# Performance work log

Measured on AMD Instinct MI355X. Metric: run time of the kernel, lower is better.

The kernel has to match this reference:

```python
import jax, jax.numpy as jnp
import numpy as np

B, QL, CL = 4, 256, 512
XD, ED, DIM, YD = 128, 128, 128, 16


def setup_inputs() -> dict:
    key = jax.random.key(0)
    ks = jax.random.split(key, 9)
    s = lambda fan_in: 1.0 / np.sqrt(fan_in)
    return {
        "q": jax.random.normal(ks[0], (B, QL, XD), jnp.float32),
        "f_embed": jax.random.normal(ks[1], (B, CL, ED), jnp.float32),
        "att_logits": jax.random.normal(ks[2], (B, QL, CL), jnp.float32),
        # layer 1 of concat-MLP, split into per-branch blocks (same math as concat@W1)
        "W1q": jax.random.normal(ks[3], (XD, DIM), jnp.float32) * s(XD + ED),
        "W1f": jax.random.normal(ks[4], (ED, DIM), jnp.float32) * s(XD + ED),
        "b1": jnp.zeros((DIM,), jnp.float32),
        "W2": jax.random.normal(ks[5], (DIM, DIM), jnp.float32) * s(DIM),
        "b2": jnp.zeros((DIM,), jnp.float32),
        "Wout": jax.random.normal(ks[6], (DIM, 2 * YD), jnp.float32) * s(DIM),
        "bout": jnp.zeros((2 * YD,), jnp.float32),
    }


def reference(q, f_embed, att_logits, W1q, W1f, b1, W2, b2, Wout, bout):
    # First layer: concat([tile(q), tile(f)]) @ W1 == q@W1q (+) f@W1f broadcast-added.
    qp = jnp.einsum("bqd,dh->bqh", q, W1q)            # [B,Q,H]
    fp = jnp.einsum("bcd,dh->bch", f_embed, W1f)      # [B,C,H]
    h = jax.nn.relu(qp[:, :, None, :] + fp[:, None, :, :] + b1)   # [B,Q,C,H]
    h = jax.nn.relu(jnp.einsum("bqch,hk->bqck", h, W2) + b2)      # [B,Q,C,H]
    out = jnp.einsum("bqch,hy->bqcy", h, Wout) + bout             # [B,Q,C,2Y]
    mu, s = jnp.split(out, 2, axis=-1)                            # [B,Q,C,Y] each
    sigma = jax.nn.softplus(jnp.maximum(-15.0, s))
    # MixtureSameFamily(Categorical(att_logits), MVNDiag(mu, sigma)).sample()
    kcat, keps = jax.random.split(jax.random.key(1))
    idx = jax.random.categorical(kcat, att_logits, axis=-1)       # [B,Q]
    gather = lambda t: jnp.take_along_axis(t, idx[:, :, None, None], axis=2)[:, :, 0, :]
    mu_sel, sig_sel = gather(mu), gather(sigma)                   # [B,Q,Y]
    eps = jax.random.normal(keps, mu_sel.shape, mu_sel.dtype)
    y_hat = mu_sel + sig_sel * eps                                # [B,Q,Y]
    return y_hat
```

## Files before the change

kernel.cpp:

```cpp
#include <hip/hip_runtime.h>
#include <stdint.h>

#define Bc   4
#define QLc  256
#define CLc  512
#define Dc   128
#define YDc  16
#define NROW (Bc * QLc)

__device__ __forceinline__ uint32_t rotl32(uint32_t x, int d) {
  return (x << d) | (x >> (32 - d));
}

__device__ __forceinline__ void tf2x32(uint32_t k0, uint32_t k1, uint32_t x0,
                                       uint32_t x1, uint32_t& o0, uint32_t& o1) {
  const uint32_t k2 = k0 ^ k1 ^ 0x1BD11BDAu;
  uint32_t v0 = x0 + k0, v1 = x1 + k1;
  v0 += v1; v1 = rotl32(v1, 13); v1 ^= v0;
  v0 += v1; v1 = rotl32(v1, 15); v1 ^= v0;
  v0 += v1; v1 = rotl32(v1, 26); v1 ^= v0;
  v0 += v1; v1 = rotl32(v1, 6);  v1 ^= v0;
  v0 += k1; v1 += k2 + 1u;
  v0 += v1; v1 = rotl32(v1, 17); v1 ^= v0;
  v0 += v1; v1 = rotl32(v1, 29); v1 ^= v0;
  v0 += v1; v1 = rotl32(v1, 16); v1 ^= v0;
  v0 += v1; v1 = rotl32(v1, 24); v1 ^= v0;
  v0 += k2; v1 += k0 + 2u;
  v0 += v1; v1 = rotl32(v1, 13); v1 ^= v0;
  v0 += v1; v1 = rotl32(v1, 15); v1 ^= v0;
  v0 += v1; v1 = rotl32(v1, 26); v1 ^= v0;
  v0 += v1; v1 = rotl32(v1, 6);  v1 ^= v0;
  v0 += k0; v1 += k1 + 3u;
  v0 += v1; v1 = rotl32(v1, 17); v1 ^= v0;
  v0 += v1; v1 = rotl32(v1, 29); v1 ^= v0;
  v0 += v1; v1 = rotl32(v1, 16); v1 ^= v0;
  v0 += v1; v1 = rotl32(v1, 24); v1 ^= v0;
  v0 += k1; v1 += k2 + 4u;
  v0 += v1; v1 = rotl32(v1, 13); v1 ^= v0;
  v0 += v1; v1 = rotl32(v1, 15); v1 ^= v0;
  v0 += v1; v1 = rotl32(v1, 26); v1 ^= v0;
  v0 += v1; v1 = rotl32(v1, 6);  v1 ^= v0;
  v0 += k2; v1 += k0 + 5u;
  o0 = v0; o1 = v1;
}

__device__ __forceinline__ void subkeys(uint32_t& ck0, uint32_t& ck1,
                                        uint32_t& ek0, uint32_t& ek1) {
  tf2x32(0u, 1u, 0u, 0u, ck0, ck1);
  tf2x32(0u, 1u, 0u, 1u, ek0, ek1);
}

__device__ __forceinline__ uint32_t rbits(uint32_t k0, uint32_t k1, uint32_t i) {
  uint32_t o0, o1;
  tf2x32(k0, k1, 0u, i, o0, o1);
  return o0 ^ o1;
}

__device__ __forceinline__ float bits_to_unit(uint32_t bits) {
  return __uint_as_float((bits >> 9) | 0x3f800000u) - 1.0f;
}

__device__ __forceinline__ float erfinv_f(float x) {
  float w = -logf((1.0f - x) * (1.0f + x));
  float p;
  if (w < 5.0f) {
    w -= 2.5f;
    p = 2.81022636e-08f;
    p = fmaf(p, w, 3.43273939e-07f);
    p = fmaf(p, w, -3.5233877e-06f);
    p = fmaf(p, w, -4.39150654e-06f);
    p = fmaf(p, w, 0.00021858087f);
    p = fmaf(p, w, -0.00125372503f);
    p = fmaf(p, w, -0.00417768164f);
    p = fmaf(p, w, 0.246640727f);
    p = fmaf(p, w, 1.50140941f);
  } else {
    w = sqrtf(w) - 3.0f;
    p = -0.000200214257f;
    p = fmaf(p, w, 0.000100950558f);
    p = fmaf(p, w, 0.00134934322f);
    p = fmaf(p, w, -0.00367342844f);
    p = fmaf(p, w, 0.00573950773f);
    p = fmaf(p, w, -0.0076224613f);
    p = fmaf(p, w, 0.00943887047f);
    p = fmaf(p, w, 1.00167406f);
    p = fmaf(p, w, 2.83297682f);
  }
  return p * x;
}

__global__ __launch_bounds__(256) void k_fused(
    const float* __restrict__ q, const float* __restrict__ f,
    const float* __restrict__ logits, const float* __restrict__ W1q,
    const float* __restrict__ W1f, const float* __restrict__ b1,
    const float* __restrict__ W2, const float* __restrict__ b2,
    const float* __restrict__ Wout, const float* __restrict__ bout,
    float* __restrict__ out) {
  const int tid = threadIdx.x;
  const int r   = tid >> 7;
  const int l   = tid & 127;
  const int row = blockIdx.x * 2 + r;
  const int b   = row >> 8;

  __shared__ float sx[2][Dc];
  __shared__ float sh[2][Dc];
  __shared__ float sv[256];
  __shared__ int   si[256];
  __shared__ float spart[2][4][32];
  __shared__ float so[2][32];
  __shared__ int   sc[2];

  const float qv = q[row * Dc + l];

  uint32_t ck0, ck1, ek0, ek1;
  subkeys(ck0, ck1, ek0, ek1);

  float best = -3.4e38f;
  int bi = 1 << 30;
#pragma unroll
  for (int j = 0; j < 4; ++j) {
    const int c = l + j * 128;
    const uint32_t i = (uint32_t)(row * CLc + c);
    const uint32_t bits = rbits(ck0, ck1, i);
    const float fl = bits_to_unit(bits);
    const float u = fmaxf(1.17549435e-38f, fl);
    const float g = -logf(-logf(u));
    const float val = g + logits[i];
    if (val > best || (val == best && c < bi)) { best = val; bi = c; }
  }
  sv[tid] = best; si[tid] = bi;
  __syncthreads();
  for (int s = 64; s > 0; s >>= 1) {
    if (l < s) {
      const int a0 = r * 128 + l, a1 = a0 + s;
      const float v2 = sv[a1];
      const int i2 = si[a1];
      if (v2 > sv[a0] || (v2 == sv[a0] && i2 < si[a0])) {
        sv[a0] = v2; si[a0] = i2;
      }
    }
    __syncthreads();
  }
  if (l == 0) sc[r] = si[r * 128];

  sx[r][l] = qv;
  __syncthreads();
  float acc1 = 0.0f;
  for (int h = 0; h < Dc; ++h) acc1 = fmaf(sx[r][h], W1q[h * Dc + l], acc1);

  const int csel = sc[r];
  const float fv = f[(b * CLc + csel) * Dc + l];
  __syncthreads();
  sx[r][l] = fv;
  __syncthreads();
  float accf = 0.0f;
  for (int h = 0; h < Dc; ++h) accf = fmaf(sx[r][h], W1f[h * Dc + l], accf);

  sh[r][l] = fmaxf(acc1 + accf + b1[l], 0.0f);
  __syncthreads();

  float acc2 = b2[l];
  for (int h = 0; h < Dc; ++h) acc2 = fmaf(sh[r][h], W2[h * Dc + l], acc2);
  __syncthreads();
  sh[r][l] = fmaxf(acc2, 0.0f);
  __syncthreads();

  {
    const int k  = tid & 31;
    const int rr = (tid >> 5) & 1;
    const int g  = tid >> 6;
    float p = 0.0f;
#pragma unroll
    for (int hh = 0; hh < 32; ++hh) {
      const int h = g * 32 + hh;
      p = fmaf(sh[rr][h], Wout[h * 32 + k], p);
    }
    spart[rr][g][k] = p;
  }
  __syncthreads();
  if (tid < 64) {
    const int rr = tid >> 5, k = tid & 31;
    so[rr][k] = bout[k] + spart[rr][0][k] + spart[rr][1][k] +
                spart[rr][2][k] + spart[rr][3][k];
  }
  __syncthreads();

  if (tid < 32) {
    const int rr = tid >> 4, y = tid & 15;
    const int orow = blockIdx.x * 2 + rr;
    const float mu = so[rr][y];
    const float s  = so[rr][16 + y];
    const float sm = fmaxf(-15.0f, s);
    const float sigma = fmaxf(sm, 0.0f) + log1pf(expf(-fabsf(sm)));

    const uint32_t i = (uint32_t)(orow * YDc + y);
    const uint32_t bits = rbits(ek0, ek1, i);
    const float fl = bits_to_unit(bits);
    const float lo = -0.999999940395355224609375f;
    const float prod = __fmul_rn(fl, 2.0f);
    const float u = fmaxf(lo, __fadd_rn(prod, lo));
    const float eps = 1.4142135623730951f * erfinv_f(u);
    out[orow * YDc + y] = mu + sigma * eps;
  }
}

extern "C" void kernel_launch(void* const* d_in, const int* in_sizes, int n_in,
                              void* d_out, int out_size, void* d_ws, size_t ws_size,
                              hipStream_t stream) {
  const float* q      = (const float*)d_in[0];
  const float* f      = (const float*)d_in[1];
  const float* logits = (const float*)d_in[2];
  const float* W1q    = (const float*)d_in[3];
  const float* W1f    = (const float*)d_in[4];
  const float* b1     = (const float*)d_in[5];
  const float* W2     = (const float*)d_in[6];
  const float* b2     = (const float*)d_in[7];
  const float* Wout   = (const float*)d_in[8];
  const float* bout   = (const float*)d_in[9];
  float* out = (float*)d_out;

  k_fused<<<dim3(NROW / 2), dim3(256), 0, stream>>>(
      q, f, logits, W1q, W1f, b1, W2, b2, Wout, bout, out);
}
```

Before: 85.47 us.

## Process four rows per block, use wave shuffles for argmax, and hoist eps generation

Each block now handles four rows with 512 threads instead of two with 256. The shared-memory tree reduction for the categorical argmax becomes a 64-lane shuffle reduction plus one cross-wave combine. The Gaussian noise is computed early so it overlaps with other work. The mat-vec loops read the activation vector as float4 from shared memory, and the final combine and softplus are merged into one phase using a shuffle. Together these cut barrier count and redundant weight loads per row, at the cost of fewer blocks (256) and larger blocks.

New measurement: 118.9 us. 1.39x slower.

```diff
diff --git a/kernel.cpp b/kernel.cpp
--- a/kernel.cpp
+++ b/kernel.cpp
@@ -7,6 +7,8 @@
 #define Dc   128
 #define YDc  16
 #define NROW (Bc * QLc)
+#define RPB  4
+#define TPB  512
 
 __device__ __forceinline__ uint32_t rotl32(uint32_t x, int d) {
   return (x << d) | (x >> (32 - d));
@@ -89,7 +91,7 @@
   return p * x;
 }
 
-__global__ __launch_bounds__(256) void k_fused(
+__global__ __launch_bounds__(TPB) void k_fused(
     const float* __restrict__ q, const float* __restrict__ f,
     const float* __restrict__ logits, const float* __restrict__ W1q,
     const float* __restrict__ W1f, const float* __restrict__ b1,
@@ -99,21 +101,41 @@
   const int tid = threadIdx.x;
   const int r   = tid >> 7;
   const int l   = tid & 127;
-  const int row = blockIdx.x * 2 + r;
+  const int row = blockIdx.x * RPB + r;
   const int b   = row >> 8;
 
-  __shared__ float sx[2][Dc];
-  __shared__ float sh[2][Dc];
-  __shared__ float sv[256];
-  __shared__ int   si[256];
-  __shared__ float spart[2][4][32];
-  __shared__ float so[2][32];
-  __shared__ int   sc[2];
+  __shared__ __align__(16) float sxq[RPB][Dc];
+  __shared__ __align__(16) float sxf[RPB][Dc];
+  __shared__ __align__(16) float sh1[RPB][Dc];
+  __shared__ __align__(16) float sh2[RPB][Dc];
+  __shared__ float spart[RPB][4][32];
+  __shared__ float swv[8];
+  __shared__ int   swi[8];
+  __shared__ float seps[64];
 
   const float qv = q[row * Dc + l];
 
   uint32_t ck0, ck1, ek0, ek1;
   subkeys(ck0, ck1, ek0, ek1);
+
+  if (tid < 64) {
+    const int rr = tid >> 4, y = tid & 15;
+    const int orow = blockIdx.x * RPB + rr;
+    const uint32_t i = (uint32_t)(orow * YDc + y);
+    const uint32_t bits = rbits(ek0, ek1, i);
+    const float fl = bits_to_unit(bits);
+    const float lo = -0.999999940395355224609375f;
+    const float prod = __fmul_rn(fl, 2.0f);
+    const float u = fmaxf(lo, __fadd_rn(prod, lo));
+    seps[tid] = 1.4142135623730951f * erfinv_f(u);
+  }
+
+  sxq[r][l] = qv;
+
+  float lgv[4];
+#pragma unroll
+  for (int j = 0; j < 4; ++j)
+    lgv[j] = logits[(uint32_t)(row * CLc + (l + j * 128))];
 
   float best = -3.4e38f;
   int bi = 1 << 30;
@@ -125,82 +147,102 @@
     const float fl = bits_to_unit(bits);
     const float u = fmaxf(1.17549435e-38f, fl);
     const float g = -logf(-logf(u));
-    const float val = g + logits[i];
+    const float val = g + lgv[j];
     if (val > best || (val == best && c < bi)) { best = val; bi = c; }
   }
-  sv[tid] = best; si[tid] = bi;
-  __syncthreads();
-  for (int s = 64; s > 0; s >>= 1) {
-    if (l < s) {
-      const int a0 = r * 128 + l, a1 = a0 + s;
-      const float v2 = sv[a1];
-      const int i2 = si[a1];
-      if (v2 > sv[a0] || (v2 == sv[a0] && i2 < si[a0])) {
-        sv[a0] = v2; si[a0] = i2;
-      }
-    }
-    __syncthreads();
-  }
-  if (l == 0) sc[r] = si[r * 128];
-
-  sx[r][l] = qv;
-  __syncthreads();
+#pragma unroll
+  for (int s = 1; s < 64; s <<= 1) {
+    const float ov = __shfl_xor(best, s, 64);
+    const int   oi = __shfl_xor(bi, s, 64);
+    if (ov > best || (ov == best && oi < bi)) { best = ov; bi = oi; }
+  }
+  if ((tid & 63) == 0) { swv[tid >> 6] = best; swi[tid >> 6] = bi; }
+  __syncthreads();
+
+  int csel;
+  {
+    const float v0 = swv[2 * r], v1 = swv[2 * r + 1];
+    const int   i0 = swi[2 * r], i1 = swi[2 * r + 1];
+    csel = (v1 > v0 || (v1 == v0 && i1 < i0)) ? i1 : i0;
+  }
+  const float fv = f[(b * CLc + csel) * Dc + l];
+
   float acc1 = 0.0f;
-  for (int h = 0; h < Dc; ++h) acc1 = fmaf(sx[r][h], W1q[h * Dc + l], acc1);
-
-  const int csel = sc[r];
-  const float fv = f[(b * CLc + csel) * Dc + l];
-  __syncthreads();
-  sx[r][l] = fv;
-  __syncthreads();
+  {
+    const float4* xp = (const float4*)sxq[r];
+#pragma unroll
+    for (int h4 = 0; h4 < 32; ++h4) {
+      const float4 xv = xp[h4];
+      const int h = h4 * 4;
+      acc1 = fmaf(xv.x, W1q[(h + 0) * Dc + l], acc1);
+      acc1 = fmaf(xv.y, W1q[(h + 1) * Dc + l], acc1);
+      acc1 = fmaf(xv.z, W1q[(h + 2) * Dc + l], acc1);
+      acc1 = fmaf(xv.w, W1q[(h + 3) * Dc + l], acc1);
+    }
+  }
+
+  sxf[r][l] = fv;
+  __syncthreads();
+
   float accf = 0.0f;
-  for (int h = 0; h < Dc; ++h) accf = fmaf(sx[r][h], W1f[h * Dc + l], accf);
-
-  sh[r][l] = fmaxf(acc1 + accf + b1[l], 0.0f);
+  {
+    const float4* xp = (const float4*)sxf[r];
+#pragma unroll
+    for (int h4 = 0; h4 < 32; ++h4) {
+      const float4 xv = xp[h4];
+      const int h = h4 * 4;
+      accf = fmaf(xv.x, W1f[(h + 0) * Dc + l], accf);
+      accf = fmaf(xv.y, W1f[(h + 1) * Dc + l], accf);
+      accf = fmaf(xv.z, W1f[(h + 2) * Dc + l], accf);
+      accf = fmaf(xv.w, W1f[(h + 3) * Dc + l], accf);
+    }
+  }
+
+  sh1[r][l] = fmaxf(acc1 + accf + b1[l], 0.0f);
   __syncthreads();
 
   float acc2 = b2[l];
-  for (int h = 0; h < Dc; ++h) acc2 = fmaf(sh[r][h], W2[h * Dc + l], acc2);
-  __syncthreads();
-  sh[r][l] = fmaxf(acc2, 0.0f);
+  {
+    const float4* xp = (const float4*)sh1[r];
+#pragma unroll
+    for (int h4 = 0; h4 < 32; ++h4) {
+      const float4 xv = xp[h4];
+      const int h = h4 * 4;
+      acc2 = fmaf(xv.x, W2[(h + 0) * Dc + l], acc2);
+      acc2 = fmaf(xv.y, W2[(h + 1) * Dc + l], acc2);
+      acc2 = fmaf(xv.z, W2[(h + 2) * Dc + l], acc2);
+      acc2 = fmaf(xv.w, W2[(h + 3) * Dc + l], acc2);
+    }
+  }
+  sh2[r][l] = fmaxf(acc2, 0.0f);
   __syncthreads();
 
   {
     const int k  = tid & 31;
-    const int rr = (tid >> 5) & 1;
-    const int g  = tid >> 6;
+    const int rr = (tid >> 5) & 3;
+    const int g  = tid >> 7;
     float p = 0.0f;
 #pragma unroll
     for (int hh = 0; hh < 32; ++hh) {
       const int h = g * 32 + hh;
-      p = fmaf(sh[rr][h], Wout[h * 32 + k], p);
+      p = fmaf(sh2[rr][h], Wout[h * 32 + k], p);
     }
     spart[rr][g][k] = p;
   }
   __syncthreads();
-  if (tid < 64) {
+
+  if (tid < 128) {
     const int rr = tid >> 5, k = tid & 31;
-    so[rr][k] = bout[k] + spart[rr][0][k] + spart[rr][1][k] +
-                spart[rr][2][k] + spart[rr][3][k];
-  }
-  __syncthreads();
-
-  if (tid < 32) {
-    const int rr = tid >> 4, y = tid & 15;
-    const int orow = blockIdx.x * 2 + rr;
-    const float mu = so[rr][y];
-    const float s  = so[rr][16 + y];
-    const float sm = fmaxf(-15.0f, s);
-    const float sigma = fmaxf(sm, 0.0f) + log1pf(expf(-fabsf(sm)));
-
-    const uint32_t i = (uint32_t)(orow * YDc + y);
-    const uint32_t bits = rbits(ek0, ek1, i);
-    const float fl = bits_to_unit(bits);
-    const float lo = -0.999999940395355224609375f;
-    const float prod = __fmul_rn(fl, 2.0f);
-    const float u = fmaxf(lo, __fadd_rn(prod, lo));
-    const float eps = 1.4142135623730951f * erfinv_f(u);
-    out[orow * YDc + y] = mu + sigma * eps;
+    const int orow = blockIdx.x * RPB + rr;
+    const float ov = bout[k] + spart[rr][0][k] + spart[rr][1][k] +
+                     spart[rr][2][k] + spart[rr][3][k];
+    const float sv_ = __shfl(ov, (tid & 63) + 16, 64);
+    if (k < 16) {
+      const float mu = ov;
+      const float sm = fmaxf(-15.0f, sv_);
+      const float sigma = fmaxf(sm, 0.0f) + log1pf(expf(-fabsf(sm)));
+      out[orow * YDc + k] = mu + sigma * seps[rr * 16 + k];
+    }
   }
 }
 
@@ -219,6 +261,6 @@
   const float* bout   = (const float*)d_in[9];
   float* out = (float*)d_out;
 
-  k_fused<<<dim3(NROW / 2), dim3(256), 0, stream>>>(
+  k_fused<<<dim3(NROW / RPB), dim3(TPB), 0, stream>>>(
       q, f, logits, W1q, W1f, b1, W2, b2, Wout, bout, out);
 }
```
